# Kernel tuning notes

Hardware: AMD Instinct MI355X
Metric: run time of the kernel (lower is better)

Reference implementation:

```python
import jax, jax.numpy as jnp
import numpy as np

B, T, D, H = 4, 8192, 512, 512


def log_g(x):
    # log of the 'continuous relu-ish' gate: log(relu(x)+0.5) for x>=0, -softplus(-x) otherwise
    return jnp.where(x >= 0, jnp.log(jax.nn.relu(x) + 0.5), -jax.nn.softplus(-x))


def setup_inputs() -> dict:
    key = jax.random.key(0)
    ks = jax.random.split(key, 8)
    s = 1.0 / np.sqrt(D)
    return {
        "x": jax.random.normal(ks[0], (B, T, D), dtype=jnp.float32),
        "h_0": jax.random.normal(ks[1], (B, 1, H), dtype=jnp.float32),
        "W_f": jax.random.normal(ks[2], (D, H), dtype=jnp.float32) * s,
        "b_f": jnp.zeros((H,), dtype=jnp.float32),
        "W_i": jax.random.normal(ks[3], (D, H), dtype=jnp.float32) * s,
        "b_i": jnp.zeros((H,), dtype=jnp.float32),
        "W_h": jax.random.normal(ks[4], (D, H), dtype=jnp.float32) * s,
        "b_h": jnp.zeros((H,), dtype=jnp.float32),
    }


def reference(x, h_0, W_f, b_f, W_i, b_i, W_h, b_h):
    # three dense gate projections: [B,T,H]
    f_pre = jnp.einsum("btd,dh->bth", x, W_f) + b_f
    i_pre = jnp.einsum("btd,dh->bth", x, W_i) + b_i
    h_pre = jnp.einsum("btd,dh->bth", x, W_h) + b_h

    diff = jax.nn.softplus(-f_pre) - jax.nn.softplus(-i_pre)
    log_f = -jax.nn.softplus(diff)            # log forget gate  [B,T,H]
    log_i = -jax.nn.softplus(-diff)           # log input  gate  [B,T,H]

    log_h0 = log_g(h_0)                       # [B,1,H]
    log_tilde_h = log_g(h_pre)                # [B,T,H]
    log_values = jnp.concatenate([log_h0, log_i + log_tilde_h], axis=1)  # [B,T+1,H]

    # a_star[t] = sum_{s<=t} log_f[s], with a leading zero for the h_0 slot
    a_star = jnp.pad(jnp.cumsum(log_f, axis=1), ((0, 0), (1, 0), (0, 0)))  # [B,T+1,H]
    # stable parallel scan in log space
    log_h = a_star + jax.lax.cumlogsumexp(log_values - a_star, axis=1)     # [B,T+1,H]
    return jnp.exp(log_h)
```

## Files before the change

kernel.cpp:

```cpp
#include <hip/hip_runtime.h>
#include <hip/hip_bf16.h>

#define B_ 4
#define T_ 8192
#define D_ 512
#define H_ 512
#define M_ (B_ * T_)
#define CHUNK_ 128
#define SUB_ 32
#define NSUB_ (T_ / SUB_)
#define SEQS_ (B_ * H_)

typedef __attribute__((ext_vector_type(8))) short bf16x8;
typedef __attribute__((ext_vector_type(4))) float f32x4;

__device__ __forceinline__ unsigned short f2bf(float x) {
  union { float f; unsigned int u; } c; c.f = x;
  unsigned int u = c.u;
  unsigned int r = (u + 0x7fffu + ((u >> 16) & 1u)) >> 16;
  return (unsigned short)r;
}
__device__ __forceinline__ float bf2f(unsigned short h) {
  union { unsigned int u; float f; } c; c.u = ((unsigned int)h) << 16;
  return c.f;
}

__device__ __forceinline__ void gll16(const void* g, void* l) {
  __builtin_amdgcn_global_load_lds(
      (const __attribute__((address_space(1))) unsigned int*)g,
      (__attribute__((address_space(3))) unsigned int*)l, 16, 0, 0);
}

__global__ void wt_convert(const float* __restrict__ Wf, const float* __restrict__ Wi,
                           const float* __restrict__ Wh, unsigned short* __restrict__ Wt) {
  int e = blockIdx.x * 256 + threadIdx.x;
  int g = e >> 16;
  int rem = e & 65535;
  int n = rem >> 7;
  int k4 = (rem & 127) * 4;
  const float* W = (g == 0) ? Wf : (g == 1) ? Wi : Wh;
  ushort4 o;
  o.x = f2bf(W[(k4 + 0) * H_ + n]);
  o.y = f2bf(W[(k4 + 1) * H_ + n]);
  o.z = f2bf(W[(k4 + 2) * H_ + n]);
  o.w = f2bf(W[(k4 + 3) * H_ + n]);
  *(ushort4*)(Wt + ((size_t)g * H_ + n) * D_ + k4) = o;
}

__global__ void x_convert(const float* __restrict__ x, unsigned short* __restrict__ xb) {
  size_t i = ((size_t)blockIdx.x * 256 + threadIdx.x) * 8;
  float4 a = *(const float4*)(x + i);
  float4 b = *(const float4*)(x + i + 4);
  ushort4 ha; ha.x = f2bf(a.x); ha.y = f2bf(a.y); ha.z = f2bf(a.z); ha.w = f2bf(a.w);
  ushort4 hb; hb.x = f2bf(b.x); hb.y = f2bf(b.y); hb.z = f2bf(b.z); hb.w = f2bf(b.w);
  *(ushort4*)(xb + i) = ha;
  *(ushort4*)(xb + i + 4) = hb;
}

__global__ __launch_bounds__(256, 2)
void gemm_gates(const unsigned short* __restrict__ xb, const unsigned short* __restrict__ Wt,
                const float* __restrict__ bF, const float* __restrict__ bI,
                const float* __restrict__ bH, unsigned int* __restrict__ AV,
                float* __restrict__ Fc, float* __restrict__ Sc) {
  __shared__ unsigned short xs[128 * 64];
  __shared__ unsigned short wsm[3 * 64 * 64];
  __shared__ unsigned int avs[128 * 64];

  const int tid = threadIdx.x;
  const int hb = blockIdx.x;
  const int m0 = blockIdx.y * 128;
  const int n0 = hb * 64;
  const int wave = tid >> 6;
  const int lane = tid & 63;
  const int wm = (wave & 1) * 64;
  const int wn = (wave >> 1) * 32;
  const int l16 = lane & 15;
  const int quad = lane >> 4;

  const int lrow = lane >> 3;
  const int lch = (lane & 7) ^ lrow;

  int xoff[4];
  #pragma unroll
  for (int j = 0; j < 4; ++j) {
    const int gx = wave * 4 + j;
    xoff[j] = (m0 + gx * 8 + lrow) * D_ + lch * 8;
  }
  int woff[6], wdst[6];
  #pragma unroll
  for (int q = 0; q < 6; ++q) {
    const int gw = wave * 6 + q;
    const int g = gw >> 3, rg = gw & 7;
    woff[q] = (g * H_ + n0 + rg * 8 + lrow) * D_ + lch * 8;
    wdst[q] = g * 4096 + rg * 512;
  }

  f32x4 acc[3][4][2];
  #pragma unroll
  for (int g = 0; g < 3; ++g)
    #pragma unroll
    for (int mi = 0; mi < 4; ++mi)
      #pragma unroll
      for (int ni = 0; ni < 2; ++ni)
        acc[g][mi][ni] = (f32x4){0.f, 0.f, 0.f, 0.f};

  #pragma unroll 1
  for (int kb = 0; kb < D_; kb += 64) {
    #pragma unroll
    for (int j = 0; j < 4; ++j)
      gll16(xb + xoff[j] + kb, xs + (wave * 4 + j) * 512);
    #pragma unroll
    for (int q = 0; q < 6; ++q)
      gll16(Wt + woff[q] + kb, wsm + wdst[q]);
    __syncthreads();

    #pragma unroll
    for (int kk = 0; kk < 64; kk += 32) {
      const int kc = kk >> 3;
      bf16x8 af[4];
      #pragma unroll
      for (int mi = 0; mi < 4; ++mi) {
        const int r = wm + mi * 16 + l16;
        af[mi] = *(const bf16x8*)(xs + r * 64 + ((kc + quad) ^ (r & 7)) * 8);
      }
      bf16x8 bfr[3][2];
      #pragma unroll
      for (int g = 0; g < 3; ++g)
        #pragma unroll
        for (int ni = 0; ni < 2; ++ni) {
          const int r = wn + ni * 16 + l16;
          bfr[g][ni] = *(const bf16x8*)(wsm + g * 4096 + r * 64 + ((kc + quad) ^ (r & 7)) * 8);
        }
      #pragma unroll
      for (int g = 0; g < 3; ++g)
        #pragma unroll
        for (int mi = 0; mi < 4; ++mi)
          #pragma unroll
          for (int ni = 0; ni < 2; ++ni)
            acc[g][mi][ni] = __builtin_amdgcn_mfma_f32_16x16x32_bf16(
                af[mi], bfr[g][ni], acc[g][mi][ni], 0, 0, 0);
    }
    __syncthreads();
  }

  const size_t avbase = ((size_t)blockIdx.y * 8 + hb) * (CHUNK_ * 64);
  #pragma unroll
  for (int ni = 0; ni < 2; ++ni) {
    const int col = n0 + wn + ni * 16 + l16;
    const int hl = wn + ni * 16 + l16;
    const float bfv = bF[col], biv = bI[col], bhv = bH[col];
    #pragma unroll
    for (int mi = 0; mi < 4; ++mi) {
      const int tb = wm + mi * 16 + quad * 4;
      #pragma unroll
      for (int r = 0; r < 4; ++r) {
        float fp = acc[0][mi][ni][r] + bfv;
        float ip = acc[1][mi][ni][r] + biv;
        float hp = acc[2][mi][ni][r] + bhv;
        fp = fminf(fmaxf(fp, -30.f), 30.f);
        ip = fminf(fmaxf(ip, -30.f), 30.f);
        hp = fminf(fmaxf(hp, -30.f), 30.f);
        const float Ef = __expf(-fp);
        const float Ei = __expf(-ip);
        const float rr2 = 1.f / (2.f + Ef + Ei);
        const float fgate = (1.f + Ei) * rr2;
        const float igate = (1.f + Ef) * rr2;
        float gval;
        if (hp >= 0.f) gval = hp + 0.5f;
        else gval = 1.f / (1.f + __expf(-hp));
        const float vval = igate * gval;
        const int t = tb + r;
        const unsigned int packed =
            (unsigned int)f2bf(fgate) | ((unsigned int)f2bf(vval) << 16);
        AV[avbase + (size_t)t * 64 + hl] = packed;
        avs[t * 64 + (hl ^ (((t >> 2) & 3) << 4))] = packed;
      }
    }
  }
  __syncthreads();

  const int seg = tid >> 6;
  const int shl = tid & 63;
  float F = 1.f, S = 0.f;
  #pragma unroll 8
  for (int t = seg * SUB_; t < seg * SUB_ + SUB_; ++t) {
    const unsigned int w = avs[t * 64 + (shl ^ (((t >> 2) & 3) << 4))];
    const float a = bf2f((unsigned short)(w & 0xffffu));
    const float v = bf2f((unsigned short)(w >> 16));
    F *= a;
    S = fmaf(a, S, v);
  }
  const int bb = m0 >> 13;
  const int cc = (m0 & 8191) >> 7;
  const int sidx = cc * 4 + seg;
  const int seq = bb * 512 + n0 + shl;
  Fc[(size_t)sidx * SEQS_ + seq] = F;
  Sc[(size_t)sidx * SEQS_ + seq] = S;
}

__global__ void scan_pass2(const float* __restrict__ h0, const float* __restrict__ Fc,
                           const float* __restrict__ Sc, float* __restrict__ Hin,
                           float* __restrict__ out) {
  const int s = blockIdx.x * 256 + threadIdx.x;
  const int b = s >> 9;
  const int h = s & 511;
  float x = h0[s];
  float hcur = (x >= 0.f) ? (x + 0.5f) : (1.f / (1.f + __expf(-x)));
  out[(size_t)(b * (T_ + 1)) * H_ + h] = hcur;
  #pragma unroll 8
  for (int c = 0; c < NSUB_; ++c) {
    Hin[(size_t)c * SEQS_ + s] = hcur;
    hcur = fmaf(Fc[(size_t)c * SEQS_ + s], hcur, Sc[(size_t)c * SEQS_ + s]);
  }
}

__global__ void scan_pass3(const unsigned int* __restrict__ AV,
                           const float* __restrict__ Hin, float* __restrict__ out) {
  const int gid = blockIdx.x * 256 + threadIdx.x;
  const int hl = gid & 63;
  const int rest = gid >> 6;
  const int hbi = rest & 7;
  const int sub = (rest >> 3) & 3;
  const int c = (rest >> 5) & 63;
  const int b = rest >> 11;
  const unsigned int* p = AV + (size_t)((b * 64 + c) * 8 + hbi) * (CHUNK_ * 64)
                             + sub * SUB_ * 64 + hl;
  float* o = out + ((size_t)(b * (T_ + 1) + c * CHUNK_ + sub * SUB_ + 1) * H_)
                 + hbi * 64 + hl;
  const int seq = b * 512 + hbi * 64 + hl;
  float hcur = Hin[(size_t)(c * 4 + sub) * SEQS_ + seq];
  #pragma unroll 8
  for (int t = 0; t < SUB_; ++t) {
    const unsigned int w = p[t * 64];
    const float a = bf2f((unsigned short)(w & 0xffffu));
    const float v = bf2f((unsigned short)(w >> 16));
    hcur = fmaf(a, hcur, v);
    o[(size_t)t * H_] = hcur;
  }
}

extern "C" void kernel_launch(void* const* d_in, const int* in_sizes, int n_in,
                              void* d_out, int out_size, void* d_ws, size_t ws_size,
                              hipStream_t stream) {
  const float* x  = (const float*)d_in[0];
  const float* h0 = (const float*)d_in[1];
  const float* Wf = (const float*)d_in[2];
  const float* bF = (const float*)d_in[3];
  const float* Wi = (const float*)d_in[4];
  const float* bI = (const float*)d_in[5];
  const float* Wh = (const float*)d_in[6];
  const float* bH = (const float*)d_in[7];
  float* out = (float*)d_out;

  char* ws = (char*)d_ws;
  size_t off = 0;
  unsigned int* AV = (unsigned int*)(ws + off);      off += (size_t)M_ * H_ * 4;
  unsigned short* xbf = (unsigned short*)(ws + off); off += (size_t)M_ * D_ * 2;
  unsigned short* Wt = (unsigned short*)(ws + off);  off += (size_t)3 * H_ * D_ * 2;
  float* Fc  = (float*)(ws + off); off += (size_t)NSUB_ * SEQS_ * 4;
  float* Sc  = (float*)(ws + off); off += (size_t)NSUB_ * SEQS_ * 4;
  float* Hin = (float*)(ws + off); off += (size_t)NSUB_ * SEQS_ * 4;

  wt_convert<<<(3 * H_ * D_ / 4) / 256, 256, 0, stream>>>(Wf, Wi, Wh, Wt);
  x_convert<<<(M_ * D_) / (256 * 8), 256, 0, stream>>>(x, xbf);
  gemm_gates<<<dim3(H_ / 64, M_ / 128), 256, 0, stream>>>(xbf, Wt, bF, bI, bH, AV, Fc, Sc);
  scan_pass2<<<SEQS_ / 256, 256, 0, stream>>>(h0, Fc, Sc, Hin, out);
  scan_pass3<<<(SEQS_ * (T_ / SUB_)) / 256, 256, 0, stream>>>(AV, Hin, out);
}
```

Before: 259.8 us.

## Split scan pass1 out of GEMM, parallelize pass2, merge convert kernels

Moves the per-subchunk scan reduction out of the GEMM epilogue into a separate scan_pass1 kernel that reads AV back from global memory. This drops the 32KB avs LDS buffer and a barrier from the GEMM, which may help occupancy. scan_pass2 becomes a two-level scan per block: 32 sequences per block, with Fc/Sc staged in LDS, so the serial 256-step chain over only 2048 threads is replaced by more parallel work. The two convert kernels are fused into one launch. The cost is an extra launch and an extra full read of AV.

After: 229.8 us. 1.13x faster.

```diff
diff --git a/kernel.cpp b/kernel.cpp
--- a/kernel.cpp
+++ b/kernel.cpp
@@ -31,40 +31,36 @@
       (__attribute__((address_space(3))) unsigned int*)l, 16, 0, 0);
 }
 
-__global__ void wt_convert(const float* __restrict__ Wf, const float* __restrict__ Wi,
-                           const float* __restrict__ Wh, unsigned short* __restrict__ Wt) {
-  int e = blockIdx.x * 256 + threadIdx.x;
-  int g = e >> 16;
-  int rem = e & 65535;
-  int n = rem >> 7;
-  int k4 = (rem & 127) * 4;
-  const float* W = (g == 0) ? Wf : (g == 1) ? Wi : Wh;
-  ushort4 o;
-  o.x = f2bf(W[(k4 + 0) * H_ + n]);
-  o.y = f2bf(W[(k4 + 1) * H_ + n]);
-  o.z = f2bf(W[(k4 + 2) * H_ + n]);
-  o.w = f2bf(W[(k4 + 3) * H_ + n]);
-  *(ushort4*)(Wt + ((size_t)g * H_ + n) * D_ + k4) = o;
-}
-
-__global__ void x_convert(const float* __restrict__ x, unsigned short* __restrict__ xb) {
-  size_t i = ((size_t)blockIdx.x * 256 + threadIdx.x) * 8;
-  float4 a = *(const float4*)(x + i);
-  float4 b = *(const float4*)(x + i + 4);
-  ushort4 ha; ha.x = f2bf(a.x); ha.y = f2bf(a.y); ha.z = f2bf(a.z); ha.w = f2bf(a.w);
-  ushort4 hb; hb.x = f2bf(b.x); hb.y = f2bf(b.y); hb.z = f2bf(b.z); hb.w = f2bf(b.w);
-  *(ushort4*)(xb + i) = ha;
-  *(ushort4*)(xb + i + 4) = hb;
+__global__ void convert_all(const float* __restrict__ x, const float* __restrict__ Wf,
+                            const float* __restrict__ Wi, const float* __restrict__ Wh,
+                            unsigned short* __restrict__ xbf, unsigned short* __restrict__ Wt) {
+  const int gid = blockIdx.x * 256 + threadIdx.x;
+  const size_t i = (size_t)gid * 4;
+  const float4 a = *(const float4*)(x + i);
+  ushort4 hv;
+  hv.x = f2bf(a.x); hv.y = f2bf(a.y); hv.z = f2bf(a.z); hv.w = f2bf(a.w);
+  *(ushort4*)(xbf + i) = hv;
+  if (gid < 3 * H_ * D_ / 4) {
+    const int g = gid >> 16;
+    const int rem = gid & 65535;
+    const int n = rem >> 7;
+    const int k4 = (rem & 127) * 4;
+    const float* W = (g == 0) ? Wf : (g == 1) ? Wi : Wh;
+    ushort4 o;
+    o.x = f2bf(W[(k4 + 0) * H_ + n]);
+    o.y = f2bf(W[(k4 + 1) * H_ + n]);
+    o.z = f2bf(W[(k4 + 2) * H_ + n]);
+    o.w = f2bf(W[(k4 + 3) * H_ + n]);
+    *(ushort4*)(Wt + ((size_t)g * H_ + n) * D_ + k4) = o;
+  }
 }
 
 __global__ __launch_bounds__(256, 2)
 void gemm_gates(const unsigned short* __restrict__ xb, const unsigned short* __restrict__ Wt,
                 const float* __restrict__ bF, const float* __restrict__ bI,
-                const float* __restrict__ bH, unsigned int* __restrict__ AV,
-                float* __restrict__ Fc, float* __restrict__ Sc) {
+                const float* __restrict__ bH, unsigned int* __restrict__ AV) {
   __shared__ unsigned short xs[128 * 64];
   __shared__ unsigned short wsm[3 * 64 * 64];
-  __shared__ unsigned int avs[128 * 64];
 
   const int tid = threadIdx.x;
   const int hb = blockIdx.x;
@@ -76,16 +72,13 @@
   const int wn = (wave >> 1) * 32;
   const int l16 = lane & 15;
   const int quad = lane >> 4;
-
   const int lrow = lane >> 3;
   const int lch = (lane & 7) ^ lrow;
 
   int xoff[4];
   #pragma unroll
-  for (int j = 0; j < 4; ++j) {
-    const int gx = wave * 4 + j;
-    xoff[j] = (m0 + gx * 8 + lrow) * D_ + lch * 8;
-  }
+  for (int j = 0; j < 4; ++j)
+    xoff[j] = (m0 + (wave * 4 + j) * 8 + lrow) * D_ + lch * 8;
   int woff[6], wdst[6];
   #pragma unroll
   for (int q = 0; q < 6; ++q) {
@@ -146,8 +139,8 @@
   const size_t avbase = ((size_t)blockIdx.y * 8 + hb) * (CHUNK_ * 64);
   #pragma unroll
   for (int ni = 0; ni < 2; ++ni) {
-    const int col = n0 + wn + ni * 16 + l16;
     const int hl = wn + ni * 16 + l16;
+    const int col = n0 + hl;
     const float bfv = bF[col], biv = bI[col], bhv = bH[col];
     #pragma unroll
     for (int mi = 0; mi < 4; ++mi) {
@@ -169,48 +162,96 @@
         if (hp >= 0.f) gval = hp + 0.5f;
         else gval = 1.f / (1.f + __expf(-hp));
         const float vval = igate * gval;
-        const int t = tb + r;
-        const unsigned int packed =
+        AV[avbase + (size_t)(tb + r) * 64 + hl] =
             (unsigned int)f2bf(fgate) | ((unsigned int)f2bf(vval) << 16);
-        AV[avbase + (size_t)t * 64 + hl] = packed;
-        avs[t * 64 + (hl ^ (((t >> 2) & 3) << 4))] = packed;
       }
     }
   }
-  __syncthreads();
-
-  const int seg = tid >> 6;
-  const int shl = tid & 63;
+}
+
+__global__ void scan_pass1(const unsigned int* __restrict__ AV,
+                           float* __restrict__ Fc, float* __restrict__ Sc) {
+  const int gid = blockIdx.x * 256 + threadIdx.x;
+  const int hl = gid & 63;
+  const int rest = gid >> 6;
+  const int hbi = rest & 7;
+  const int sub = (rest >> 3) & 3;
+  const int c = (rest >> 5) & 63;
+  const int b = rest >> 11;
+  const unsigned int* p = AV + (size_t)((b * 64 + c) * 8 + hbi) * (CHUNK_ * 64)
+                             + sub * SUB_ * 64 + hl;
   float F = 1.f, S = 0.f;
   #pragma unroll 8
-  for (int t = seg * SUB_; t < seg * SUB_ + SUB_; ++t) {
-    const unsigned int w = avs[t * 64 + (shl ^ (((t >> 2) & 3) << 4))];
+  for (int t = 0; t < SUB_; ++t) {
+    const unsigned int w = p[t * 64];
     const float a = bf2f((unsigned short)(w & 0xffffu));
     const float v = bf2f((unsigned short)(w >> 16));
     F *= a;
     S = fmaf(a, S, v);
   }
-  const int bb = m0 >> 13;
-  const int cc = (m0 & 8191) >> 7;
-  const int sidx = cc * 4 + seg;
-  const int seq = bb * 512 + n0 + shl;
+  const int sidx = c * 4 + sub;
+  const int seq = b * 512 + hbi * 64 + hl;
   Fc[(size_t)sidx * SEQS_ + seq] = F;
   Sc[(size_t)sidx * SEQS_ + seq] = S;
 }
 
-__global__ void scan_pass2(const float* __restrict__ h0, const float* __restrict__ Fc,
-                           const float* __restrict__ Sc, float* __restrict__ Hin,
-                           float* __restrict__ out) {
-  const int s = blockIdx.x * 256 + threadIdx.x;
-  const int b = s >> 9;
-  const int h = s & 511;
-  float x = h0[s];
-  float hcur = (x >= 0.f) ? (x + 0.5f) : (1.f / (1.f + __expf(-x)));
-  out[(size_t)(b * (T_ + 1)) * H_ + h] = hcur;
+__global__ __launch_bounds__(256, 2)
+void scan_pass2(const float* __restrict__ h0, const float* __restrict__ Fc,
+                const float* __restrict__ Sc, float* __restrict__ Hin,
+                float* __restrict__ out) {
+  __shared__ float Fs[NSUB_ * 32];
+  __shared__ float Ss[NSUB_ * 32];
+  __shared__ float Fg[8 * 32], Sg[8 * 32], Hg[8 * 32];
+
+  const int tid = threadIdx.x;
+  const int seq0 = blockIdx.x * 32;
+
   #pragma unroll 8
-  for (int c = 0; c < NSUB_; ++c) {
-    Hin[(size_t)c * SEQS_ + s] = hcur;
-    hcur = fmaf(Fc[(size_t)c * SEQS_ + s], hcur, Sc[(size_t)c * SEQS_ + s]);
+  for (int i = tid; i < NSUB_ * 32; i += 256) {
+    const int sub = i >> 5;
+    const int sl = i & 31;
+    Fs[i] = Fc[(size_t)sub * SEQS_ + seq0 + sl];
+    Ss[i] = Sc[(size_t)sub * SEQS_ + seq0 + sl];
+  }
+  __syncthreads();
+
+  const int g = tid >> 5;
+  const int sl = tid & 31;
+  {
+    float F = 1.f, S = 0.f;
+    #pragma unroll 8
+    for (int j = 0; j < 32; ++j) {
+      const int idx = (g * 32 + j) * 32 + sl;
+      S = fmaf(Fs[idx], S, Ss[idx]);
+      F *= Fs[idx];
+    }
+    Fg[g * 32 + sl] = F;
+    Sg[g * 32 + sl] = S;
+  }
+  __syncthreads();
+
+  if (tid < 32) {
+    const int seq = seq0 + tid;
+    const int b = seq >> 9;
+    const int h = seq & 511;
+    const float xv = h0[seq];
+    float hcur = (xv >= 0.f) ? (xv + 0.5f) : (1.f / (1.f + __expf(-xv)));
+    out[(size_t)(b * (T_ + 1)) * H_ + h] = hcur;
+    #pragma unroll
+    for (int gg = 0; gg < 8; ++gg) {
+      Hg[gg * 32 + tid] = hcur;
+      hcur = fmaf(Fg[gg * 32 + tid], hcur, Sg[gg * 32 + tid]);
+    }
+  }
+  __syncthreads();
+
+  float h = Hg[g * 32 + sl];
+  #pragma unroll 8
+  for (int j = 0; j < 32; ++j) {
+    const int sub = g * 32 + j;
+    const int idx = sub * 32 + sl;
+    Hin[(size_t)sub * SEQS_ + seq0 + sl] = h;
+    h = fmaf(Fs[idx], h, Ss[idx]);
   }
 }
 
@@ -261,9 +302,9 @@
   float* Sc  = (float*)(ws + off); off += (size_t)NSUB_ * SEQS_ * 4;
   float* Hin = (float*)(ws + off); off += (size_t)NSUB_ * SEQS_ * 4;
 
-  wt_convert<<<(3 * H_ * D_ / 4) / 256, 256, 0, stream>>>(Wf, Wi, Wh, Wt);
-  x_convert<<<(M_ * D_) / (256 * 8), 256, 0, stream>>>(x, xbf);
-  gemm_gates<<<dim3(H_ / 64, M_ / 128), 256, 0, stream>>>(xbf, Wt, bF, bI, bH, AV, Fc, Sc);
-  scan_pass2<<<SEQS_ / 256, 256, 0, stream>>>(h0, Fc, Sc, Hin, out);
-  scan_pass3<<<(SEQS_ * (T_ / SUB_)) / 256, 256, 0, stream>>>(AV, Hin, out);
-}
+  convert_all<<<(M_ * D_ / 4) / 256, 256, 0, stream>>>(x, Wf, Wi, Wh, xbf, Wt);
+  gemm_gates<<<dim3(H_ / 64, M_ / 128), 256, 0, stream>>>(xbf, Wt, bF, bI, bH, AV);
+  scan_pass1<<<(SEQS_ * NSUB_) / 256, 256, 0, stream>>>(AV, Fc, Sc);
+  scan_pass2<<<SEQS_ / 32, 256, 0, stream>>>(h0, Fc, Sc, Hin, out);
+  scan_pass3<<<(SEQS_ * NSUB_) / 256, 256, 0, stream>>>(AV, Hin, out);
+}
```
